# Kernel optimization log

Measured on AMD Instinct MI355X. Metric: run time of the kernel, lower is better.

The kernel has to match this reference:

```python
import jax, jax.numpy as jnp
import numpy as np

N, L, FEAT = 16, 4096, 512
DIN = 21 * 14 * 3 + FEAT  # 1394
EPS = 1e-6


def setup_inputs() -> dict:
    key = jax.random.key(0)
    ks = jax.random.split(key, 12)

    def lin_w(k, i, o):
        return (jax.random.normal(k, (i, o), jnp.float32) / np.sqrt(i)).astype(jnp.float32)

    return {
        "aa": jax.random.randint(ks[0], (N, L), 0, 21),
        "pos14": jax.random.normal(ks[1], (N, L, 14, 3), jnp.float32),
        "atom_mask": jax.random.bernoulli(ks[2], 0.9, (N, L, 14)),
        "embed": (jax.random.normal(ks[3], (21, FEAT), jnp.float32) * 0.02),
        "w1": lin_w(ks[4], DIN, 2 * FEAT),
        "b1": jnp.zeros((2 * FEAT,), jnp.float32),
        "w2": lin_w(ks[5], 2 * FEAT, FEAT),
        "b2": jnp.zeros((FEAT,), jnp.float32),
        "w3": lin_w(ks[6], FEAT, FEAT),
        "b3": jnp.zeros((FEAT,), jnp.float32),
        "w4": lin_w(ks[7], FEAT, FEAT),
        "b4": jnp.zeros((FEAT,), jnp.float32),
    }


def _normalize(v):
    return v / (jnp.linalg.norm(v, axis=-1, keepdims=True) + EPS)


def reference(aa, pos14, atom_mask, embed, w1, b1, w2, b2, w3, b3, w4, b4):
    n, l = aa.shape
    # --- frame construction: center=CA (atom 1), p1=C (atom 2), p2=N (atom 0)
    center = pos14[:, :, 1]
    v1 = pos14[:, :, 2] - center
    e1 = _normalize(v1)
    v2 = pos14[:, :, 0] - center
    u2 = v2 - jnp.sum(e1 * v2, axis=-1, keepdims=True) * e1  # Gram-Schmidt
    e2 = _normalize(u2)
    e3 = jnp.cross(e1, e2)
    R = jnp.stack([e1, e2, e3], axis=-1)  # (N,L,3,3), columns [e1,e2,e3]

    # --- global_to_local: p = R^T (q - t)
    q = pos14 - center[:, :, None, :]            # (N,L,14,3)
    crd14 = jnp.einsum('nlij,nlai->nlaj', R, q)  # (N,L,14,3)
    crd14 = jnp.where(atom_mask[..., None], crd14, 0.0)

    # --- one-hot residue placement (equivalent to the (N,L,21,14,3) expand+where)
    onehot = jax.nn.one_hot(aa, 21, dtype=crd14.dtype)             # (N,L,21)
    crd_feat = (onehot[..., None] * crd14.reshape(n, l, 1, 14 * 3))
    crd_feat = crd_feat.reshape(n, l, 21 * 14 * 3)                  # (N,L,882)

    aa_feat = embed[aa]                                             # (N,L,FEAT)
    h = jnp.concatenate([crd_feat, aa_feat], axis=-1)               # (N,L,1394)
    h = jax.nn.relu(h @ w1 + b1)
    h = jax.nn.relu(h @ w2 + b2)
    h = jax.nn.relu(h @ w3 + b3)
    return h @ w4 + b4
```

## Files before the change

kernel.cpp:

```cpp
#include <hip/hip_runtime.h>
#include <hip/hip_bf16.h>


typedef __attribute__((ext_vector_type(8))) short short8;
typedef __attribute__((ext_vector_type(4))) float floatx4;

#define TOKENS 65536
#define FEATD 512
#define L1OUT 1024
#define NAA 21
#define EPSF 1e-6f
#define ORDER_N 66880

static __device__ __forceinline__ unsigned short f2bf(float f) {
  union { float f; unsigned int u; } v; v.f = f;
  unsigned int u = v.u;
  return (unsigned short)((u + 0x7FFFu + ((u >> 16) & 1u)) >> 16);
}

#define GLDS16(g, l) __builtin_amdgcn_global_load_lds(                        \
    (const __attribute__((address_space(1))) unsigned int*)(g),               \
    (__attribute__((address_space(3))) unsigned int*)(l), 16, 0, 0)

__global__ void k_init(int* __restrict__ order, int* __restrict__ counts) {
  int i = blockIdx.x * 256 + threadIdx.x;
  if (i < ORDER_N) order[i] = -1;
  if (i < 64) counts[i] = 0;
}

__global__ void k_detect(const unsigned int* __restrict__ mask, int* __restrict__ flag) {
  unsigned int v = mask[threadIdx.x];
  int b = 0;
  if (v == 0x3F800000u) b = 2;
  else if (v > 1u) b = 1;
  if (b) atomicOr(flag, b);
}

__global__ void k_feat(const float* __restrict__ pos14, const int* __restrict__ aa,
                       const void* __restrict__ maskp, float* __restrict__ crd,
                       int* __restrict__ counts) {
  __shared__ int hist[NAA];
  const int tid = threadIdx.x;
  if (tid < NAA) hist[tid] = 0;
  __syncthreads();
  const int t = blockIdx.x * 256 + tid;
  const int fl = counts[32];
  const float* p = pos14 + (size_t)t * 42;
  float px[14], py[14], pz[14];
#pragma unroll
  for (int a = 0; a < 14; ++a) { px[a] = p[a*3]; py[a] = p[a*3+1]; pz[a] = p[a*3+2]; }
  float cx = px[1], cy = py[1], cz = pz[1];
  float v1x = px[2]-cx, v1y = py[2]-cy, v1z = pz[2]-cz;
  float n1 = sqrtf(v1x*v1x + v1y*v1y + v1z*v1z);
  float i1 = 1.f / (n1 + EPSF);
  float e1x = v1x*i1, e1y = v1y*i1, e1z = v1z*i1;
  float v2x = px[0]-cx, v2y = py[0]-cy, v2z = pz[0]-cz;
  float d12 = e1x*v2x + e1y*v2y + e1z*v2z;
  float u2x = v2x - d12*e1x, u2y = v2y - d12*e1y, u2z = v2z - d12*e1z;
  float n2 = sqrtf(u2x*u2x + u2y*u2y + u2z*u2z);
  float i2 = 1.f / (n2 + EPSF);
  float e2x = u2x*i2, e2y = u2y*i2, e2z = u2z*i2;
  float e3x = e1y*e2z - e1z*e2y;
  float e3y = e1z*e2x - e1x*e2z;
  float e3z = e1x*e2y - e1y*e2x;
  float* o = crd + (size_t)t * 42;
#pragma unroll
  for (int a = 0; a < 14; ++a) {
    bool mv;
    size_t mi = (size_t)t * 14 + a;
    if (fl & 2)      mv = ((const float*)maskp)[mi] != 0.f;
    else if (fl & 1) mv = ((const unsigned char*)maskp)[mi] != 0;
    else             mv = ((const int*)maskp)[mi] != 0;
    float qx = px[a]-cx, qy = py[a]-cy, qz = pz[a]-cz;
    o[a*3+0] = mv ? (e1x*qx + e1y*qy + e1z*qz) : 0.f;
    o[a*3+1] = mv ? (e2x*qx + e2y*qy + e2z*qz) : 0.f;
    o[a*3+2] = mv ? (e3x*qx + e3y*qy + e3z*qz) : 0.f;
  }
  atomicAdd(&hist[aa[t]], 1);
  __syncthreads();
  if (tid < NAA && hist[tid]) atomicAdd(&counts[tid], hist[tid]);
}

__global__ void k_offsets(const int* __restrict__ counts, int* __restrict__ cnt2) {
  if (threadIdx.x == 0) {
    int run = 0;
    for (int a = 0; a < NAA; ++a) { cnt2[a] = run; run += ((counts[a] + 63) >> 6) << 6; }
  }
}

__global__ void k_scatter(const int* __restrict__ aa, int* __restrict__ cnt2,
                          int* __restrict__ order) {
  __shared__ int lh[NAA], base[NAA];
  const int tid = threadIdx.x;
  if (tid < NAA) lh[tid] = 0;
  __syncthreads();
  const int t = blockIdx.x * 256 + tid;
  const int a = aa[t];
  const int r = atomicAdd(&lh[a], 1);
  __syncthreads();
  if (tid < NAA) base[tid] = lh[tid] ? atomicAdd(&cnt2[tid], lh[tid]) : 0;
  __syncthreads();
  order[base[a] + r] = t;
}

__global__ void k_T1(const float* __restrict__ embed, const float* __restrict__ w1,
                     const float* __restrict__ b1, float* __restrict__ T1) {
  int idx = blockIdx.x * 256 + threadIdx.x;
  int a = idx >> 10, c = idx & 1023;
  float acc = b1[c];
  const float* e = embed + a * FEATD;
#pragma unroll 8
  for (int k = 0; k < FEATD; ++k)
    acc += e[k] * w1[(size_t)(882 + k) * L1OUT + c];
  T1[idx] = acc;
}

__global__ void k_transpose(const float* __restrict__ W, unsigned short* __restrict__ WT,
                            int kbits, int N) {
  int idx = blockIdx.x * 256 + threadIdx.x;
  int K = 1 << kbits;
  int n = idx >> kbits, k = idx & (K - 1);
  WT[(size_t)n * K + k] = f2bf(W[(size_t)k * N + n]);
}

__global__ void k_layer1(const int* __restrict__ order, const int* __restrict__ aa_g,
                         const float* __restrict__ crd, const float* __restrict__ w1,
                         const float* __restrict__ T1, unsigned short* __restrict__ h1) {
  __shared__ int tokens[64];
  __shared__ int s_aa;
  __shared__ float crdl[64 * 42];
  __shared__ float Wl[42 * 132];
  const int tid = threadIdx.x;
  const int pb = blockIdx.y;
  const int cc = blockIdx.x * 128;
  if (tid < 64) tokens[tid] = order[pb * 64 + tid];
  __syncthreads();
  if (tid == 0) {
    int a = -1;
    for (int i = 0; i < 64; ++i) if (tokens[i] >= 0) { a = aa_g[tokens[i]]; break; }
    s_aa = a;
  }
  __syncthreads();
  const int a = s_aa;
  if (a < 0) return;
  for (int idx = tid; idx < 64 * 42; idx += 256) {
    int pos = idx / 42, j = idx - pos * 42;
    int tok = tokens[pos];
    crdl[idx] = (tok >= 0) ? crd[(size_t)tok * 42 + j] : 0.f;
  }
  const float* wsrc = w1 + (size_t)a * 42 * L1OUT + cc;
  for (int idx = tid; idx < 42 * 128; idx += 256) {
    int j = idx >> 7, c = idx & 127;
    Wl[j * 132 + c] = wsrc[(size_t)j * L1OUT + c];
  }
  __syncthreads();
  const int posl = (tid >> 4) * 4;
  const int colb = (tid & 15) * 8;
  float acc[4][8];
  {
    const float* tb = T1 + a * L1OUT + cc + colb;
#pragma unroll
    for (int q = 0; q < 8; ++q) {
      float t = tb[q];
#pragma unroll
      for (int pp = 0; pp < 4; ++pp) acc[pp][q] = t;
    }
  }
  for (int j = 0; j < 42; ++j) {
    float4 wA = *(const float4*)&Wl[j * 132 + colb];
    float4 wB = *(const float4*)&Wl[j * 132 + colb + 4];
#pragma unroll
    for (int pp = 0; pp < 4; ++pp) {
      float cv = crdl[(posl + pp) * 42 + j];
      acc[pp][0] += cv * wA.x; acc[pp][1] += cv * wA.y;
      acc[pp][2] += cv * wA.z; acc[pp][3] += cv * wA.w;
      acc[pp][4] += cv * wB.x; acc[pp][5] += cv * wB.y;
      acc[pp][6] += cv * wB.z; acc[pp][7] += cv * wB.w;
    }
  }
#pragma unroll
  for (int pp = 0; pp < 4; ++pp) {
    int tok = tokens[posl + pp];
    if (tok < 0) continue;
    unsigned short o8[8];
#pragma unroll
    for (int q = 0; q < 8; ++q) o8[q] = f2bf(fmaxf(acc[pp][q], 0.f));
    *(uint4*)&h1[(size_t)tok * L1OUT + cc + colb] = *(const uint4*)o8;
  }
}

template<int K, bool RELU, bool OUTBF16>
__global__ void k_gemm(const unsigned short* __restrict__ A,
                       const unsigned short* __restrict__ BT,
                       const float* __restrict__ bias, void* __restrict__ outp) {
  constexpr int N = 512;
  __shared__ unsigned short Al[128 * 64];
  __shared__ unsigned short Bl[128 * 64];
  const int tid = threadIdx.x;
  const int lane = tid & 63;
  const int wid = tid >> 6;
  const int wm = (wid & 1) * 64;
  const int wn = (wid >> 1) * 64;
  const int m0 = blockIdx.y * 128;
  const int n0 = blockIdx.x * 128;
  const int srow = wid * 32;
  const int lrow = lane >> 3;
  const int gcol = ((lane & 7) ^ lrow) * 8;
  floatx4 acc[4][4] = {};
  for (int k0 = 0; k0 < K; k0 += 64) {
#pragma unroll
    for (int i = 0; i < 4; ++i) {
      const int row = srow + i * 8;
      GLDS16(&A [(size_t)(m0 + row + lrow) * K + k0 + gcol], &Al[row * 64]);
      GLDS16(&BT[(size_t)(n0 + row + lrow) * K + k0 + gcol], &Bl[row * 64]);
    }
    __syncthreads();
#pragma unroll
    for (int kk = 0; kk < 2; ++kk) {
      short8 af[4], bf[4];
      const int kc = kk * 4 + (lane >> 4);
      const int swz = (kc ^ (lane & 7)) * 8;
#pragma unroll
      for (int i = 0; i < 4; ++i) {
        af[i] = *(const short8*)&Al[(wm + i * 16 + (lane & 15)) * 64 + swz];
        bf[i] = *(const short8*)&Bl[(wn + i * 16 + (lane & 15)) * 64 + swz];
      }
#pragma unroll
      for (int i = 0; i < 4; ++i)
#pragma unroll
        for (int j = 0; j < 4; ++j)
          acc[i][j] = __builtin_amdgcn_mfma_f32_16x16x32_bf16(af[i], bf[j], acc[i][j], 0, 0, 0);
    }
    __syncthreads();
  }
#pragma unroll
  for (int i = 0; i < 4; ++i) {
    int rbase = m0 + wm + i * 16 + ((lane >> 4) << 2);
#pragma unroll
    for (int j = 0; j < 4; ++j) {
      int col = n0 + wn + j * 16 + (lane & 15);
      float bv = bias[col];
#pragma unroll
      for (int r = 0; r < 4; ++r) {
        float v = acc[i][j][r] + bv;
        if (RELU) v = fmaxf(v, 0.f);
        size_t off = (size_t)(rbase + r) * N + col;
        if (OUTBF16) ((unsigned short*)outp)[off] = f2bf(v);
        else ((float*)outp)[off] = v;
      }
    }
  }
}

extern "C" void kernel_launch(void* const* d_in, const int* in_sizes, int n_in,
                              void* d_out, int out_size, void* d_ws, size_t ws_size,
                              hipStream_t stream) {
  const int*   aa    = (const int*)d_in[0];
  const float* pos14 = (const float*)d_in[1];
  const void*  mask  = d_in[2];
  const float* embed = (const float*)d_in[3];
  const float* w1    = (const float*)d_in[4];
  const float* b1    = (const float*)d_in[5];
  const float* w2    = (const float*)d_in[6];
  const float* b2    = (const float*)d_in[7];
  const float* w3    = (const float*)d_in[8];
  const float* b3    = (const float*)d_in[9];
  const float* w4    = (const float*)d_in[10];
  const float* b4    = (const float*)d_in[11];

  char* ws = (char*)d_ws;
  size_t o = 0;
  auto alloc = [&](size_t b) { size_t r = o; o += (b + 255) & ~(size_t)255; return r; };
  unsigned short* w2T = (unsigned short*)(ws + alloc((size_t)512 * 1024 * 2));
  unsigned short* w3T = (unsigned short*)(ws + alloc((size_t)512 * 512 * 2));
  unsigned short* w4T = (unsigned short*)(ws + alloc((size_t)512 * 512 * 2));
  float* T1   = (float*)(ws + alloc((size_t)NAA * 1024 * 4));
  float* crd  = (float*)(ws + alloc((size_t)TOKENS * 42 * 4));
  int* counts = (int*)(ws + alloc(64 * 4));
  int* cnt2   = (int*)(ws + alloc(64 * 4));
  int* order  = (int*)(ws + alloc((size_t)ORDER_N * 4));
  unsigned short* h1 = (unsigned short*)(ws + alloc((size_t)TOKENS * 1024 * 2));
  unsigned short* h2 = (unsigned short*)(ws + alloc((size_t)TOKENS * 512 * 2));
  unsigned short* h3 = h1;

  k_init<<<262, 256, 0, stream>>>(order, counts);
  k_detect<<<1, 256, 0, stream>>>((const unsigned int*)mask, &counts[32]);
  k_transpose<<<2048, 256, 0, stream>>>(w2, w2T, 10, 512);
  k_transpose<<<1024, 256, 0, stream>>>(w3, w3T, 9, 512);
  k_transpose<<<1024, 256, 0, stream>>>(w4, w4T, 9, 512);
  k_T1<<<84, 256, 0, stream>>>(embed, w1, b1, T1);
  k_feat<<<256, 256, 0, stream>>>(pos14, aa, mask, crd, counts);
  k_offsets<<<1, 64, 0, stream>>>(counts, cnt2);
  k_scatter<<<256, 256, 0, stream>>>(aa, cnt2, order);
  k_layer1<<<dim3(8, 1045), 256, 0, stream>>>(order, aa, crd, w1, T1, h1);
  k_gemm<1024, true,  true ><<<dim3(4, 512), 256, 0, stream>>>(h1, w2T, b2, h2);
  k_gemm<512,  true,  true ><<<dim3(4, 512), 256, 0, stream>>>(h2, w3T, b3, h3);
  k_gemm<512,  false, false><<<dim3(4, 512), 256, 0, stream>>>(h3, w4T, b4, d_out);
}
```

Before: 522.9 us.

## Run layer-1 residue-grouped GEMM on bf16 MFMA with padded K=64 layouts

The per-residue layer-1 projection now uses bf16 MFMA. Coordinates are stored as bf16 rows padded to 64, and w1's per-residue slices are pre-transposed into bf16 K-major tiles loaded via global_load_lds with a swizzle. This replaces the scalar fp32 FMA loop and halves the coordinate traffic. In exchange it adds a w1 conversion kernel, bf16 rounding of the inputs, and output stores that are now scattered 2-byte writes instead of 16-byte vectors.

```diff
diff --git a/kernel.cpp b/kernel.cpp
--- a/kernel.cpp
+++ b/kernel.cpp
@@ -37,7 +37,7 @@
 }
 
 __global__ void k_feat(const float* __restrict__ pos14, const int* __restrict__ aa,
-                       const void* __restrict__ maskp, float* __restrict__ crd,
+                       const void* __restrict__ maskp, unsigned short* __restrict__ crdb,
                        int* __restrict__ counts) {
   __shared__ int hist[NAA];
   const int tid = threadIdx.x;
@@ -63,7 +63,7 @@
   float e3x = e1y*e2z - e1z*e2y;
   float e3y = e1z*e2x - e1x*e2z;
   float e3z = e1x*e2y - e1y*e2x;
-  float* o = crd + (size_t)t * 42;
+  unsigned short ob[64];
 #pragma unroll
   for (int a = 0; a < 14; ++a) {
     bool mv;
@@ -72,10 +72,15 @@
     else if (fl & 1) mv = ((const unsigned char*)maskp)[mi] != 0;
     else             mv = ((const int*)maskp)[mi] != 0;
     float qx = px[a]-cx, qy = py[a]-cy, qz = pz[a]-cz;
-    o[a*3+0] = mv ? (e1x*qx + e1y*qy + e1z*qz) : 0.f;
-    o[a*3+1] = mv ? (e2x*qx + e2y*qy + e2z*qz) : 0.f;
-    o[a*3+2] = mv ? (e3x*qx + e3y*qy + e3z*qz) : 0.f;
-  }
+    ob[a*3+0] = mv ? f2bf(e1x*qx + e1y*qy + e1z*qz) : 0;
+    ob[a*3+1] = mv ? f2bf(e2x*qx + e2y*qy + e2z*qz) : 0;
+    ob[a*3+2] = mv ? f2bf(e3x*qx + e3y*qy + e3z*qz) : 0;
+  }
+#pragma unroll
+  for (int k = 42; k < 64; ++k) ob[k] = 0;
+  uint4* dst = (uint4*)&crdb[(size_t)t * 64];
+#pragma unroll
+  for (int q = 0; q < 8; ++q) dst[q] = ((const uint4*)ob)[q];
   atomicAdd(&hist[aa[t]], 1);
   __syncthreads();
   if (tid < NAA && hist[tid]) atomicAdd(&counts[tid], hist[tid]);
@@ -115,6 +120,18 @@
   T1[idx] = acc;
 }
 
+__global__ void k_w1T(const float* __restrict__ w1, unsigned short* __restrict__ w1T2) {
+  int idx = blockIdx.x * 256 + threadIdx.x;
+  int a = idx >> 10, c = idx & 1023;
+  unsigned short tmp[64];
+#pragma unroll
+  for (int k = 0; k < 64; ++k)
+    tmp[k] = (k < 42) ? f2bf(w1[(size_t)(a * 42 + k) * L1OUT + c]) : 0;
+  uint4* dst = (uint4*)&w1T2[(size_t)idx * 64];
+#pragma unroll
+  for (int q = 0; q < 8; ++q) dst[q] = ((const uint4*)tmp)[q];
+}
+
 __global__ void k_transpose(const float* __restrict__ W, unsigned short* __restrict__ WT,
                             int kbits, int N) {
   int idx = blockIdx.x * 256 + threadIdx.x;
@@ -124,15 +141,18 @@
 }
 
 __global__ void k_layer1(const int* __restrict__ order, const int* __restrict__ aa_g,
-                         const float* __restrict__ crd, const float* __restrict__ w1,
+                         const unsigned short* __restrict__ crdb,
+                         const unsigned short* __restrict__ w1T2,
                          const float* __restrict__ T1, unsigned short* __restrict__ h1) {
   __shared__ int tokens[64];
   __shared__ int s_aa;
-  __shared__ float crdl[64 * 42];
-  __shared__ float Wl[42 * 132];
+  __shared__ unsigned short Al[64 * 64];
+  __shared__ unsigned short Bl[256 * 64];
   const int tid = threadIdx.x;
+  const int lane = tid & 63;
+  const int wid = tid >> 6;
   const int pb = blockIdx.y;
-  const int cc = blockIdx.x * 128;
+  const int cc = blockIdx.x * 256;
   if (tid < 64) tokens[tid] = order[pb * 64 + tid];
   __syncthreads();
   if (tid == 0) {
@@ -143,49 +163,54 @@
   __syncthreads();
   const int a = s_aa;
   if (a < 0) return;
-  for (int idx = tid; idx < 64 * 42; idx += 256) {
-    int pos = idx / 42, j = idx - pos * 42;
-    int tok = tokens[pos];
-    crdl[idx] = (tok >= 0) ? crd[(size_t)tok * 42 + j] : 0.f;
-  }
-  const float* wsrc = w1 + (size_t)a * 42 * L1OUT + cc;
-  for (int idx = tid; idx < 42 * 128; idx += 256) {
-    int j = idx >> 7, c = idx & 127;
-    Wl[j * 132 + c] = wsrc[(size_t)j * L1OUT + c];
-  }
-  __syncthreads();
-  const int posl = (tid >> 4) * 4;
-  const int colb = (tid & 15) * 8;
-  float acc[4][8];
-  {
-    const float* tb = T1 + a * L1OUT + cc + colb;
-#pragma unroll
-    for (int q = 0; q < 8; ++q) {
-      float t = tb[q];
-#pragma unroll
-      for (int pp = 0; pp < 4; ++pp) acc[pp][q] = t;
-    }
-  }
-  for (int j = 0; j < 42; ++j) {
-    float4 wA = *(const float4*)&Wl[j * 132 + colb];
-    float4 wB = *(const float4*)&Wl[j * 132 + colb + 4];
-#pragma unroll
-    for (int pp = 0; pp < 4; ++pp) {
-      float cv = crdl[(posl + pp) * 42 + j];
-      acc[pp][0] += cv * wA.x; acc[pp][1] += cv * wA.y;
-      acc[pp][2] += cv * wA.z; acc[pp][3] += cv * wA.w;
-      acc[pp][4] += cv * wB.x; acc[pp][5] += cv * wB.y;
-      acc[pp][6] += cv * wB.z; acc[pp][7] += cv * wB.w;
-    }
-  }
-#pragma unroll
-  for (int pp = 0; pp < 4; ++pp) {
-    int tok = tokens[posl + pp];
-    if (tok < 0) continue;
-    unsigned short o8[8];
-#pragma unroll
-    for (int q = 0; q < 8; ++q) o8[q] = f2bf(fmaxf(acc[pp][q], 0.f));
-    *(uint4*)&h1[(size_t)tok * L1OUT + cc + colb] = *(const uint4*)o8;
+  const int lrow = lane >> 3;
+  const int gch = (lane & 7) ^ lrow;
+#pragma unroll
+  for (int i = 0; i < 2; ++i) {
+    int row = wid * 16 + i * 8;
+    int tok = tokens[row + lrow]; if (tok < 0) tok = 0;
+    GLDS16(&crdb[(size_t)tok * 64 + gch * 8], &Al[row * 64]);
+  }
+  const unsigned short* bsrc = w1T2 + ((size_t)a * L1OUT + cc) * 64;
+#pragma unroll
+  for (int i = 0; i < 8; ++i) {
+    int row = wid * 64 + i * 8;
+    GLDS16(&bsrc[(size_t)(row + lrow) * 64 + gch * 8], &Bl[row * 64]);
+  }
+  __syncthreads();
+  const int wn = wid * 64;
+  floatx4 acc[4][4] = {};
+#pragma unroll
+  for (int kk = 0; kk < 2; ++kk) {
+    short8 af[4], bfr[4];
+    const int kc = kk * 4 + (lane >> 4);
+#pragma unroll
+    for (int i = 0; i < 4; ++i) {
+      int ar = i * 16 + (lane & 15);
+      af[i]  = *(const short8*)&Al[ar * 64 + (kc ^ (ar & 7)) * 8];
+      int br = wn + i * 16 + (lane & 15);
+      bfr[i] = *(const short8*)&Bl[br * 64 + (kc ^ (br & 7)) * 8];
+    }
+#pragma unroll
+    for (int i = 0; i < 4; ++i)
+#pragma unroll
+      for (int j = 0; j < 4; ++j)
+        acc[i][j] = __builtin_amdgcn_mfma_f32_16x16x32_bf16(af[i], bfr[j], acc[i][j], 0, 0, 0);
+  }
+#pragma unroll
+  for (int i = 0; i < 4; ++i) {
+    int tb = i * 16 + ((lane >> 4) << 2);
+#pragma unroll
+    for (int j = 0; j < 4; ++j) {
+      int colg = cc + wn + j * 16 + (lane & 15);
+      float bv = T1[a * L1OUT + colg];
+#pragma unroll
+      for (int r = 0; r < 4; ++r) {
+        int tok = tokens[tb + r];
+        if (tok < 0) continue;
+        h1[(size_t)tok * L1OUT + colg] = f2bf(fmaxf(acc[i][j][r] + bv, 0.f));
+      }
+    }
   }
 }
 
@@ -217,19 +242,19 @@
     __syncthreads();
 #pragma unroll
     for (int kk = 0; kk < 2; ++kk) {
-      short8 af[4], bf[4];
+      short8 af[4], bfr[4];
       const int kc = kk * 4 + (lane >> 4);
       const int swz = (kc ^ (lane & 7)) * 8;
 #pragma unroll
       for (int i = 0; i < 4; ++i) {
-        af[i] = *(const short8*)&Al[(wm + i * 16 + (lane & 15)) * 64 + swz];
-        bf[i] = *(const short8*)&Bl[(wn + i * 16 + (lane & 15)) * 64 + swz];
+        af[i]  = *(const short8*)&Al[(wm + i * 16 + (lane & 15)) * 64 + swz];
+        bfr[i] = *(const short8*)&Bl[(wn + i * 16 + (lane & 15)) * 64 + swz];
       }
 #pragma unroll
       for (int i = 0; i < 4; ++i)
 #pragma unroll
         for (int j = 0; j < 4; ++j)
-          acc[i][j] = __builtin_amdgcn_mfma_f32_16x16x32_bf16(af[i], bf[j], acc[i][j], 0, 0, 0);
+          acc[i][j] = __builtin_amdgcn_mfma_f32_16x16x32_bf16(af[i], bfr[j], acc[i][j], 0, 0, 0);
     }
     __syncthreads();
   }
@@ -274,8 +299,9 @@
   unsigned short* w2T = (unsigned short*)(ws + alloc((size_t)512 * 1024 * 2));
   unsigned short* w3T = (unsigned short*)(ws + alloc((size_t)512 * 512 * 2));
   unsigned short* w4T = (unsigned short*)(ws + alloc((size_t)512 * 512 * 2));
+  unsigned short* w1T2 = (unsigned short*)(ws + alloc((size_t)NAA * 1024 * 64 * 2));
   float* T1   = (float*)(ws + alloc((size_t)NAA * 1024 * 4));
-  float* crd  = (float*)(ws + alloc((size_t)TOKENS * 42 * 4));
+  unsigned short* crdb = (unsigned short*)(ws + alloc((size_t)TOKENS * 64 * 2));
   int* counts = (int*)(ws + alloc(64 * 4));
   int* cnt2   = (int*)(ws + alloc(64 * 4));
   int* order  = (int*)(ws + alloc((size_t)ORDER_N * 4));
@@ -288,11 +314,12 @@
   k_transpose<<<2048, 256, 0, stream>>>(w2, w2T, 10, 512);
   k_transpose<<<1024, 256, 0, stream>>>(w3, w3T, 9, 512);
   k_transpose<<<1024, 256, 0, stream>>>(w4, w4T, 9, 512);
+  k_w1T<<<84, 256, 0, stream>>>(w1, w1T2);
   k_T1<<<84, 256, 0, stream>>>(embed, w1, b1, T1);
-  k_feat<<<256, 256, 0, stream>>>(pos14, aa, mask, crd, counts);
+  k_feat<<<256, 256, 0, stream>>>(pos14, aa, mask, crdb, counts);
   k_offsets<<<1, 64, 0, stream>>>(counts, cnt2);
   k_scatter<<<256, 256, 0, stream>>>(aa, cnt2, order);
-  k_layer1<<<dim3(8, 1045), 256, 0, stream>>>(order, aa, crd, w1, T1, h1);
+  k_layer1<<<dim3(4, 1045), 256, 0, stream>>>(order, aa, crdb, w1T2, T1, h1);
   k_gemm<1024, true,  true ><<<dim3(4, 512), 256, 0, stream>>>(h1, w2T, b2, h2);
   k_gemm<512,  true,  true ><<<dim3(4, 512), 256, 0, stream>>>(h2, w3T, b3, h3);
   k_gemm<512,  false, false><<<dim3(4, 512), 256, 0, stream>>>(h3, w4T, b4, d_out);
```

After: 469.1 us. -10.3%, faster.
